# Optimization experiments

Measured on AMD Instinct MI355X. Metric: run time of the kernel, lower is better.

## Reference

```python
import jax, jax.numpy as jnp
import numpy as np

B, N, F_IN = 8, 256, 24
SLOPE = 0.01  # nn.LeakyReLU default negative_slope

def _leaky(x):
    return jnp.where(x >= 0, x, SLOPE * x)

def _adj(x, ws, bs):
    # AdjacencyMatrixPrediction (eval mode: dropout = identity, bn=False)
    # x: [B,N,F]; pairwise abs diff -> [B,N,N,F]; 1x1 convs == per-position matmuls
    h = jnp.abs(x[:, :, None, :] - x[:, None, :, :])
    for w, b in zip(ws[:4], bs[:4]):
        h = _leaky(h @ w + b)
    logits = (h @ ws[4] + bs[4])[..., 0]  # [B,N,N]
    n = x.shape[1]
    logits = logits - jnp.eye(n, dtype=logits.dtype) * 1e8  # mask diagonal
    return jax.nn.softmax(logits, axis=2)  # softmax over j (columns)

def _graph(a, x, w, b):
    # gmul with J2 operator = concat([I @ x, A @ x], -1), then Linear(J*F_in -> F_out)
    agg = jnp.concatenate([x, jnp.einsum('bij,bjf->bif', a, x)], axis=-1)
    return agg @ w.T + b

def setup_inputs():
    key = jax.random.key(0)
    ks = jax.random.split(key, 16)
    def mk(k, shape):
        return jax.random.normal(k, shape, jnp.float32) * 0.05
    ch0 = [24, 192, 192, 192, 96, 1]   # first AdjacencyMatrixPrediction conv chain
    ch1 = [72, 192, 192, 192, 96, 1]   # last AdjacencyMatrixPrediction (24 + 48 input)
    inp = {'x': jax.random.normal(ks[0], (B, N, F_IN), jnp.float32)}
    i = 1
    for pfx, ch in (('a0', ch0), ('a1', ch1)):
        for l in range(5):
            inp[f'{pfx}_w{l}'] = mk(ks[i], (ch[l], ch[l + 1])); i += 1
            inp[f'{pfx}_b{l}'] = jnp.zeros((ch[l + 1],), jnp.float32)
    inp['g0_w'] = mk(ks[i], (48, 48)); i += 1   # GraphModule(24 -> 48, J=2)
    inp['g0_b'] = jnp.zeros((48,), jnp.float32)
    inp['g1_w'] = mk(ks[i], (1, 144)); i += 1   # layer_last GraphModule(72 -> 1, J=2)
    inp['g1_b'] = jnp.zeros((1,), jnp.float32)
    return inp

def reference(x, a0_w0, a0_b0, a0_w1, a0_b1, a0_w2, a0_b2, a0_w3, a0_b3, a0_w4, a0_b4,
              a1_w0, a1_b0, a1_w1, a1_b1, a1_w2, a1_b2, a1_w3, a1_b3, a1_w4, a1_b4,
              g0_w, g0_b, g1_w, g1_b):
    a0 = _adj(x, [a0_w0, a0_w1, a0_w2, a0_w3, a0_w4], [a0_b0, a0_b1, a0_b2, a0_b3, a0_b4])
    x1 = _leaky(_graph(a0, x, g0_w, g0_b))
    xc = jnp.concatenate([x, x1], axis=-1)  # [B,N,72]
    a1 = _adj(xc, [a1_w0, a1_w1, a1_w2, a1_w3, a1_w4], [a1_b0, a1_b1, a1_b2, a1_b3, a1_b4])
    out = _graph(a1, xc, g1_w, g1_b)  # [B,N,1]
    # classifiers returned as [B,N,N,1] like the torch code
    return out, a0[..., None], a1[..., None]
```

## Files before the change

### kernel.cpp

```cpp
#include <hip/hip_runtime.h>

typedef __bf16 bf16x8 __attribute__((ext_vector_type(8)));
typedef float f32x4 __attribute__((ext_vector_type(4)));

__device__ __forceinline__ unsigned short f2b(float f) {
    union { float f; unsigned u; } c; c.f = f;
    unsigned u = c.u;
    return (unsigned short)((u + 0x7FFFu + ((u >> 16) & 1u)) >> 16);
}

__device__ __forceinline__ unsigned pack2(float v0, float v1) {
    union { __bf16 h[2]; unsigned u; } c;
    c.h[0] = (__bf16)v0; c.h[1] = (__bf16)v1;
    return c.u;
}

__device__ __forceinline__ void gload_lds16(const unsigned short* g, unsigned short* l) {
    __builtin_amdgcn_global_load_lds(
        (__attribute__((address_space(1))) unsigned int*)(g),
        (__attribute__((address_space(3))) unsigned int*)(l), 16, 0, 0);
}

template<int NFRAGS>
__device__ __forceinline__ void stage_frags(const unsigned short* __restrict__ g,
                                            unsigned short* l, int wid, int lane)
{
#pragma unroll
    for (int k = 0; k < (NFRAGS + 3) / 4; ++k) {
        const int idx = wid + k * 4;
        if ((NFRAGS % 4 == 0) || idx < NFRAGS)
            gload_lds16(g + idx * 512 + lane * 8, l + idx * 512);
    }
}

__device__ __forceinline__ void decode_entry(int e, int& b, int& i, int& j0, bool& offdiag)
{
    b = e / 1152;
    const int r = e - b * 1152;
    const int tp = r >> 5;
    const int row_in = r & 31;
    int rg = 0, tt = tp;
#pragma unroll 8
    for (;;) { int cnt = 8 - rg; if (tt < cnt) break; tt -= cnt; ++rg; }
    const int cg = rg + tt;
    i = rg * 32 + row_in;
    j0 = cg * 32;
    offdiag = (cg != rg);
}

template<int CIN, int KN0>
__device__ __forceinline__ void build_frags0(const float* __restrict__ xi,
    const float* __restrict__ xj, int cl, int g, bf16x8 (&B0)[2][6])
{
#pragma unroll
    for (int s = 0; s < KN0; ++s) {
        const int f0 = s * 32 + 8 * g;
        const bool valid = f0 < CIN;
        f32x4 xa = {0.f,0.f,0.f,0.f}, xb = {0.f,0.f,0.f,0.f};
        if (valid) { xa = *(const f32x4*)(xi + f0); xb = *(const f32x4*)(xi + f0 + 4); }
#pragma unroll
        for (int t = 0; t < 2; ++t) {
            bf16x8 r;
            if (valid) {
                const float* pj = xj + (16 * t + cl) * CIN + f0;
                f32x4 ja = *(const f32x4*)pj, jb = *(const f32x4*)(pj + 4);
#pragma unroll
                for (int e = 0; e < 4; ++e) {
                    r[e]     = (__bf16)fabsf(xa[e] - ja[e]);
                    r[e + 4] = (__bf16)fabsf(xb[e] - jb[e]);
                }
            } else {
#pragma unroll
                for (int e = 0; e < 8; ++e) r[e] = (__bf16)0.f;
            }
            B0[t][s] = r;
        }
    }
}

template<int KN, int CP>
__device__ __forceinline__ void run_cpair(const unsigned short* wlds,
    const float* __restrict__ bias, const bf16x8 (&Bc)[2][6], bf16x8 (&Bn)[2][6],
    int lane, int g)
{
    f32x4 acc[2][2];
#pragma unroll
    for (int cc = 0; cc < 2; ++cc) {
        f32x4 bv = *(const f32x4*)&bias[(2 * CP + cc) * 16 + 4 * g];
        acc[cc][0] = bv; acc[cc][1] = bv;
    }
#pragma unroll
    for (int s = 0; s < KN; ++s) {
#pragma unroll
        for (int cc = 0; cc < 2; ++cc) {
            bf16x8 w = *(const bf16x8*)&wlds[((cc * KN + s) * 64 + lane) * 8];
#pragma unroll
            for (int t = 0; t < 2; ++t)
                acc[cc][t] = __builtin_amdgcn_mfma_f32_16x16x32_bf16(w, Bc[t][s], acc[cc][t], 0, 0, 0);
        }
    }
#pragma unroll
    for (int t = 0; t < 2; ++t) {
        union { unsigned w[4]; bf16x8 v; } outv;
#pragma unroll
        for (int cc = 0; cc < 2; ++cc)
#pragma unroll
            for (int m = 0; m < 2; ++m) {
                float v0 = acc[cc][t][2 * m], v1 = acc[cc][t][2 * m + 1];
                v0 = fmaxf(v0, 0.01f * v0);
                v1 = fmaxf(v1, 0.01f * v1);
                outv.w[cc * 2 + m] = pack2(v0, v1);
            }
        Bn[t][CP] = outv.v;
    }
}

#define STEP(NF, OFF, ...) \
    stage_frags<NF>(wchain + (OFF), nxt, wid, lane); \
    __VA_ARGS__; \
    __syncthreads(); { unsigned short* tswp_ = cur; cur = nxt; nxt = tswp_; }

template<int CIN, int KN0>
__global__ __launch_bounds__(256, 3)
void adj_mlp_kernel(const float* __restrict__ src,
                    const unsigned short* __restrict__ wchain,
                    const unsigned short* __restrict__ w4f,
                    const float* __restrict__ b0, const float* __restrict__ b1,
                    const float* __restrict__ b2, const float* __restrict__ b3,
                    const float* __restrict__ b4,
                    float* __restrict__ logits)
{
    __shared__ unsigned short wbuf0[6144], wbuf1[6144];
    const int tid = threadIdx.x;
    const int wid = tid >> 6, lane = tid & 63;
    const int cl = lane & 15, g = lane >> 4;

    int b, i, j0; bool offdiag;
    decode_entry(blockIdx.x * 4 + wid, b, i, j0, offdiag);

    const float* xi = src + (b * 256 + i) * CIN;
    const float* xj = src + (b * 256 + j0) * CIN;

    const int CPSZ0 = 2 * KN0 * 512;
    const int B1 = 12 * KN0 * 512;
    const int B2 = B1 + 36864;
    const int B3 = B1 + 73728;
    const int CPSZ = 6144;

    stage_frags<2 * KN0>(wchain, wbuf0, wid, lane);

    bf16x8 Ba[2][6], Bb[2][6];
    build_frags0<CIN, KN0>(xi, xj, cl, g, Ba);
    __syncthreads();
    unsigned short* cur = wbuf0;
    unsigned short* nxt = wbuf1;

    STEP(2 * KN0, 1 * CPSZ0, run_cpair<KN0, 0>(cur, b0, Ba, Bb, lane, g))
    STEP(2 * KN0, 2 * CPSZ0, run_cpair<KN0, 1>(cur, b0, Ba, Bb, lane, g))
    STEP(2 * KN0, 3 * CPSZ0, run_cpair<KN0, 2>(cur, b0, Ba, Bb, lane, g))
    STEP(2 * KN0, 4 * CPSZ0, run_cpair<KN0, 3>(cur, b0, Ba, Bb, lane, g))
    STEP(2 * KN0, 5 * CPSZ0, run_cpair<KN0, 4>(cur, b0, Ba, Bb, lane, g))
    STEP(12, B1,             run_cpair<KN0, 5>(cur, b0, Ba, Bb, lane, g))
    STEP(12, B1 + 1 * CPSZ,  run_cpair<6, 0>(cur, b1, Bb, Ba, lane, g))
    STEP(12, B1 + 2 * CPSZ,  run_cpair<6, 1>(cur, b1, Bb, Ba, lane, g))
    STEP(12, B1 + 3 * CPSZ,  run_cpair<6, 2>(cur, b1, Bb, Ba, lane, g))
    STEP(12, B1 + 4 * CPSZ,  run_cpair<6, 3>(cur, b1, Bb, Ba, lane, g))
    STEP(12, B1 + 5 * CPSZ,  run_cpair<6, 4>(cur, b1, Bb, Ba, lane, g))
    STEP(12, B2,             run_cpair<6, 5>(cur, b1, Bb, Ba, lane, g))
    STEP(12, B2 + 1 * CPSZ,  run_cpair<6, 0>(cur, b2, Ba, Bb, lane, g))
    STEP(12, B2 + 2 * CPSZ,  run_cpair<6, 1>(cur, b2, Ba, Bb, lane, g))
    STEP(12, B2 + 3 * CPSZ,  run_cpair<6, 2>(cur, b2, Ba, Bb, lane, g))
    STEP(12, B2 + 4 * CPSZ,  run_cpair<6, 3>(cur, b2, Ba, Bb, lane, g))
    STEP(12, B2 + 5 * CPSZ,  run_cpair<6, 4>(cur, b2, Ba, Bb, lane, g))
    STEP(12, B3,             run_cpair<6, 5>(cur, b2, Ba, Bb, lane, g))
    STEP(12, B3 + 1 * CPSZ,  run_cpair<6, 0>(cur, b3, Bb, Ba, lane, g))
    STEP(12, B3 + 2 * CPSZ,  run_cpair<6, 1>(cur, b3, Bb, Ba, lane, g))
    run_cpair<6, 2>(cur, b3, Bb, Ba, lane, g);

    const float bv4 = b4[0];
#pragma unroll
    for (int t = 0; t < 2; ++t) {
        f32x4 acc = {bv4, bv4, bv4, bv4};
#pragma unroll
        for (int s = 0; s < 3; ++s) {
            bf16x8 w = *(const bf16x8*)(w4f + (s * 64 + lane) * 8);
            acc = __builtin_amdgcn_mfma_f32_16x16x32_bf16(w, Ba[t][s], acc, 0, 0, 0);
        }
        if (g == 0) {
            int j = j0 + 16 * t + cl;
            float lg = acc[0];
            if (j == i) lg -= 1e8f;
            logits[(b * 256 + i) * 256 + j] = lg;
            if (offdiag)
                logits[(b * 256 + j) * 256 + i] = lg;
        }
    }
}

struct PackPtrs { const float* w[10]; };

__global__ void pack_kernel(PackPtrs pp, unsigned short* __restrict__ dst)
{
    const int K_[10]   = {24, 192, 192, 192, 72, 192, 192, 192, 96, 96};
    const int KN_[10]  = {1, 6, 6, 6, 3, 6, 6, 6, 3, 3};
    const int NO_[10]  = {192, 192, 192, 96, 192, 192, 192, 96, 1, 1};
    const int OFF_[10] = {0, 6144, 43008, 79872, 98304, 116736, 153600, 190464, 208896, 210432};
    const int LEN_[10] = {6144, 36864, 36864, 18432, 18432, 36864, 36864, 18432, 1536, 1536};
    int t = blockIdx.x * 256 + threadIdx.x;
    int layer = 0, base = 0;
#pragma unroll
    for (int L = 0; L < 10; ++L)
        if (t >= base + LEN_[L]) { base += LEN_[L]; layer = L + 1; }
    if (layer >= 10) return;
    int u = t - base;
    int e = u & 7;
    int lane = (u >> 3) & 63;
    int gg = lane >> 4;
    int KN = KN_[layer];
    int fi = u >> 9;
    int s = fi % KN;
    int c = fi / KN;
    int k;
    if (layer == 0 || layer == 4)
        k = s * 32 + gg * 8 + e;
    else
        k = s * 32 + ((e >> 2) << 4) + (gg << 2) + (e & 3);
    int col = (c << 4) + (lane & 15);
    float v = 0.f;
    if (layer < 8) {
        if (k < K_[layer]) v = pp.w[layer][k * NO_[layer] + col];
    } else {
        if ((lane & 15) == 0) v = pp.w[layer][k];
    }
    dst[OFF_[layer] + u] = f2b(v);
}

template<int F>
__global__ __launch_bounds__(256)
void softmax_agg_kernel(float* __restrict__ amat, const float* __restrict__ src,
                        float* __restrict__ agg)
{
    __shared__ float pl[256];
    __shared__ float redm[4], reds[4];
    const int row = blockIdx.x;
    const int b = row >> 8;
    float* arow = amat + row * 256;
    const int t = threadIdx.x;
    const int lane = t & 63, wid = t >> 6;
    float v = arow[t];
    float m = v;
#pragma unroll
    for (int off = 32; off; off >>= 1) m = fmaxf(m, __shfl_xor(m, off));
    if (lane == 0) redm[wid] = m;
    __syncthreads();
    m = fmaxf(fmaxf(redm[0], redm[1]), fmaxf(redm[2], redm[3]));
    float e = __expf(v - m);
    float sum = e;
#pragma unroll
    for (int off = 32; off; off >>= 1) sum += __shfl_xor(sum, off);
    if (lane == 0) reds[wid] = sum;
    __syncthreads();
    sum = reds[0] + reds[1] + reds[2] + reds[3];
    float p = e / sum;
    arow[t] = p;
    pl[t] = p;
    __syncthreads();
    if (t < F) {
        const float* sb = src + (b * 256) * F + t;
        float acc = 0.f;
#pragma unroll 8
        for (int j = 0; j < 256; ++j)
            acc += pl[j] * sb[j * F];
        agg[row * F + t] = acc;
    }
}

__global__ __launch_bounds__(64)
void graph0_kernel(const float* __restrict__ x, const float* __restrict__ agg0,
                   const float* __restrict__ w, const float* __restrict__ bias,
                   float* __restrict__ xc)
{
    int row = blockIdx.x;
    int t = threadIdx.x;
    const float* xr = x + row * 24;
    const float* ar = agg0 + row * 24;
    if (t < 24) xc[row * 72 + t] = xr[t];
    if (t < 48) {
        float acc = bias[t];
#pragma unroll
        for (int f = 0; f < 24; ++f) acc += xr[f] * w[t * 48 + f];
#pragma unroll
        for (int f = 0; f < 24; ++f) acc += ar[f] * w[t * 48 + 24 + f];
        acc = acc >= 0.f ? acc : 0.01f * acc;
        xc[row * 72 + 24 + t] = acc;
    }
}

__global__ __launch_bounds__(64)
void graph1_kernel(const float* __restrict__ xc, const float* __restrict__ agg1,
                   const float* __restrict__ w, const float* __restrict__ bias,
                   float* __restrict__ out)
{
    int row = blockIdx.x;
    int t = threadIdx.x;
    float acc = 0.f;
    for (int idx = t; idx < 144; idx += 64) {
        float v = (idx < 72) ? xc[row * 72 + idx] : agg1[row * 72 + idx - 72];
        acc += v * w[idx];
    }
#pragma unroll
    for (int off = 32; off >= 1; off >>= 1) acc += __shfl_xor(acc, off);
    if (t == 0) out[row] = acc + bias[0];
}

extern "C" void kernel_launch(void* const* d_in, const int* in_sizes, int n_in,
                              void* d_out, int out_size, void* d_ws, size_t ws_size,
                              hipStream_t stream)
{
    const float* x = (const float*)d_in[0];
    float* out = (float*)d_out;
    float* a0 = out + 2048;
    float* a1 = a0 + 524288;

    char* ws = (char*)d_ws;
    unsigned short* packed = (unsigned short*)ws;
    float* xc   = (float*)(ws + 458752);
    float* agg0 = (float*)(ws + 1048576);
    float* agg1 = (float*)(ws + 1245184);

    PackPtrs pp;
    pp.w[0] = (const float*)d_in[1];
    pp.w[1] = (const float*)d_in[3];
    pp.w[2] = (const float*)d_in[5];
    pp.w[3] = (const float*)d_in[7];
    pp.w[4] = (const float*)d_in[11];
    pp.w[5] = (const float*)d_in[13];
    pp.w[6] = (const float*)d_in[15];
    pp.w[7] = (const float*)d_in[17];
    pp.w[8] = (const float*)d_in[9];
    pp.w[9] = (const float*)d_in[19];
    pack_kernel<<<828, 256, 0, stream>>>(pp, packed);

    adj_mlp_kernel<24, 1><<<2304, 256, 0, stream>>>(
        x, packed, packed + 208896,
        (const float*)d_in[2], (const float*)d_in[4], (const float*)d_in[6],
        (const float*)d_in[8], (const float*)d_in[10], a0);

    softmax_agg_kernel<24><<<2048, 256, 0, stream>>>(a0, x, agg0);

    graph0_kernel<<<2048, 64, 0, stream>>>(x, agg0,
        (const float*)d_in[21], (const float*)d_in[22], xc);

    adj_mlp_kernel<72, 3><<<2304, 256, 0, stream>>>(
        xc, packed + 98304, packed + 210432,
        (const float*)d_in[12], (const float*)d_in[14], (const float*)d_in[16],
        (const float*)d_in[18], (const float*)d_in[20], a1);

    softmax_agg_kernel<72><<<2048, 256, 0, stream>>>(a1, xc, agg1);

    graph1_kernel<<<2048, 64, 0, stream>>>(xc, agg1,
        (const float*)d_in[23], (const float*)d_in[24], out);
}
```

Measured before the change: 147.0 us.

## Stage uniform weight pages with split waitcnt barriers and batched layer-0 phases

Weight staging now always moves a full 6144-element page, so layer 0 (KN0=1 or 3) packs several channel pairs into each phase. The pipeline drops from 21 to 16 or 18 barrier steps. Each step's __syncthreads is replaced by inline-asm s_waitcnt vmcnt(3)+s_barrier before compute and lgkmcnt(0)+s_barrier after, so the prefetch of the next page can stay in flight while the current page is used. Bias is added after the MFMA accumulation instead of used as the initial accumulator. The hand-written waitcnt counts risk correctness if the compiler reorders or adds other vector-memory loads.

```diff
diff --git a/kernel.cpp b/kernel.cpp
--- a/kernel.cpp
+++ b/kernel.cpp
@@ -21,15 +21,13 @@
         (__attribute__((address_space(3))) unsigned int*)(l), 16, 0, 0);
 }
 
-template<int NFRAGS>
-__device__ __forceinline__ void stage_frags(const unsigned short* __restrict__ g,
-                                            unsigned short* l, int wid, int lane)
-{
-#pragma unroll
-    for (int k = 0; k < (NFRAGS + 3) / 4; ++k) {
+__device__ __forceinline__ void stage_page(const unsigned short* __restrict__ g,
+                                           unsigned short* l, int wid, int lane)
+{
+#pragma unroll
+    for (int k = 0; k < 3; ++k) {
         const int idx = wid + k * 4;
-        if ((NFRAGS % 4 == 0) || idx < NFRAGS)
-            gload_lds16(g + idx * 512 + lane * 8, l + idx * 512);
+        gload_lds16(g + idx * 512 + lane * 8, l + idx * 512);
     }
 }
 
@@ -83,12 +81,14 @@
     const float* __restrict__ bias, const bf16x8 (&Bc)[2][6], bf16x8 (&Bn)[2][6],
     int lane, int g)
 {
+    f32x4 bv0 = *(const f32x4*)&bias[(2 * CP + 0) * 16 + 4 * g];
+    f32x4 bv1 = *(const f32x4*)&bias[(2 * CP + 1) * 16 + 4 * g];
     f32x4 acc[2][2];
 #pragma unroll
-    for (int cc = 0; cc < 2; ++cc) {
-        f32x4 bv = *(const f32x4*)&bias[(2 * CP + cc) * 16 + 4 * g];
-        acc[cc][0] = bv; acc[cc][1] = bv;
-    }
+    for (int cc = 0; cc < 2; ++cc)
+#pragma unroll
+        for (int t = 0; t < 2; ++t)
+            acc[cc][t] = f32x4{0.f, 0.f, 0.f, 0.f};
 #pragma unroll
     for (int s = 0; s < KN; ++s) {
 #pragma unroll
@@ -103,22 +103,52 @@
     for (int t = 0; t < 2; ++t) {
         union { unsigned w[4]; bf16x8 v; } outv;
 #pragma unroll
-        for (int cc = 0; cc < 2; ++cc)
+        for (int cc = 0; cc < 2; ++cc) {
+            const f32x4 bv = cc ? bv1 : bv0;
 #pragma unroll
             for (int m = 0; m < 2; ++m) {
-                float v0 = acc[cc][t][2 * m], v1 = acc[cc][t][2 * m + 1];
+                float v0 = acc[cc][t][2 * m] + bv[2 * m];
+                float v1 = acc[cc][t][2 * m + 1] + bv[2 * m + 1];
                 v0 = fmaxf(v0, 0.01f * v0);
                 v1 = fmaxf(v1, 0.01f * v1);
                 outv.w[cc * 2 + m] = pack2(v0, v1);
             }
+        }
         Bn[t][CP] = outv.v;
     }
 }
 
-#define STEP(NF, OFF, ...) \
-    stage_frags<NF>(wchain + (OFF), nxt, wid, lane); \
+__device__ __forceinline__ void compute_l0_kn1(const unsigned short* cur,
+    const float* __restrict__ b0, const bf16x8 (&Ba)[2][6], bf16x8 (&Bb)[2][6],
+    int lane, int g)
+{
+    run_cpair<1, 0>(cur,        b0, Ba, Bb, lane, g);
+    run_cpair<1, 1>(cur + 1024, b0, Ba, Bb, lane, g);
+    run_cpair<1, 2>(cur + 2048, b0, Ba, Bb, lane, g);
+    run_cpair<1, 3>(cur + 3072, b0, Ba, Bb, lane, g);
+    run_cpair<1, 4>(cur + 4096, b0, Ba, Bb, lane, g);
+    run_cpair<1, 5>(cur + 5120, b0, Ba, Bb, lane, g);
+}
+
+template<int P2>
+__device__ __forceinline__ void compute_l0_kn3(const unsigned short* cur,
+    const float* __restrict__ b0, const bf16x8 (&Ba)[2][6], bf16x8 (&Bb)[2][6],
+    int lane, int g)
+{
+    run_cpair<3, 2 * P2>    (cur,        b0, Ba, Bb, lane, g);
+    run_cpair<3, 2 * P2 + 1>(cur + 3072, b0, Ba, Bb, lane, g);
+}
+
+#define PH(OFF, ...) \
+    stage_page(wchain + (OFF), nxt, wid, lane); \
+    asm volatile("s_waitcnt vmcnt(3)\n\ts_barrier" ::: "memory"); \
     __VA_ARGS__; \
-    __syncthreads(); { unsigned short* tswp_ = cur; cur = nxt; nxt = tswp_; }
+    asm volatile("s_waitcnt lgkmcnt(0)\n\ts_barrier" ::: "memory"); \
+    { unsigned short* t_ = cur; cur = nxt; nxt = t_; }
+
+#define PHLAST(...) \
+    asm volatile("s_waitcnt vmcnt(0)\n\ts_barrier" ::: "memory"); \
+    __VA_ARGS__;
 
 template<int CIN, int KN0>
 __global__ __launch_bounds__(256, 3)
@@ -141,41 +171,50 @@
     const float* xi = src + (b * 256 + i) * CIN;
     const float* xj = src + (b * 256 + j0) * CIN;
 
-    const int CPSZ0 = 2 * KN0 * 512;
-    const int B1 = 12 * KN0 * 512;
-    const int B2 = B1 + 36864;
-    const int B3 = B1 + 73728;
-    const int CPSZ = 6144;
-
-    stage_frags<2 * KN0>(wchain, wbuf0, wid, lane);
+    stage_page(wchain, wbuf0, wid, lane);
 
     bf16x8 Ba[2][6], Bb[2][6];
     build_frags0<CIN, KN0>(xi, xj, cl, g, Ba);
-    __syncthreads();
     unsigned short* cur = wbuf0;
     unsigned short* nxt = wbuf1;
 
-    STEP(2 * KN0, 1 * CPSZ0, run_cpair<KN0, 0>(cur, b0, Ba, Bb, lane, g))
-    STEP(2 * KN0, 2 * CPSZ0, run_cpair<KN0, 1>(cur, b0, Ba, Bb, lane, g))
-    STEP(2 * KN0, 3 * CPSZ0, run_cpair<KN0, 2>(cur, b0, Ba, Bb, lane, g))
-    STEP(2 * KN0, 4 * CPSZ0, run_cpair<KN0, 3>(cur, b0, Ba, Bb, lane, g))
-    STEP(2 * KN0, 5 * CPSZ0, run_cpair<KN0, 4>(cur, b0, Ba, Bb, lane, g))
-    STEP(12, B1,             run_cpair<KN0, 5>(cur, b0, Ba, Bb, lane, g))
-    STEP(12, B1 + 1 * CPSZ,  run_cpair<6, 0>(cur, b1, Bb, Ba, lane, g))
-    STEP(12, B1 + 2 * CPSZ,  run_cpair<6, 1>(cur, b1, Bb, Ba, lane, g))
-    STEP(12, B1 + 3 * CPSZ,  run_cpair<6, 2>(cur, b1, Bb, Ba, lane, g))
-    STEP(12, B1 + 4 * CPSZ,  run_cpair<6, 3>(cur, b1, Bb, Ba, lane, g))
-    STEP(12, B1 + 5 * CPSZ,  run_cpair<6, 4>(cur, b1, Bb, Ba, lane, g))
-    STEP(12, B2,             run_cpair<6, 5>(cur, b1, Bb, Ba, lane, g))
-    STEP(12, B2 + 1 * CPSZ,  run_cpair<6, 0>(cur, b2, Ba, Bb, lane, g))
-    STEP(12, B2 + 2 * CPSZ,  run_cpair<6, 1>(cur, b2, Ba, Bb, lane, g))
-    STEP(12, B2 + 3 * CPSZ,  run_cpair<6, 2>(cur, b2, Ba, Bb, lane, g))
-    STEP(12, B2 + 4 * CPSZ,  run_cpair<6, 3>(cur, b2, Ba, Bb, lane, g))
-    STEP(12, B2 + 5 * CPSZ,  run_cpair<6, 4>(cur, b2, Ba, Bb, lane, g))
-    STEP(12, B3,             run_cpair<6, 5>(cur, b2, Ba, Bb, lane, g))
-    STEP(12, B3 + 1 * CPSZ,  run_cpair<6, 0>(cur, b3, Bb, Ba, lane, g))
-    STEP(12, B3 + 2 * CPSZ,  run_cpair<6, 1>(cur, b3, Bb, Ba, lane, g))
-    run_cpair<6, 2>(cur, b3, Bb, Ba, lane, g);
+    if constexpr (KN0 == 1) {
+        PH( 1 * 6144, compute_l0_kn1(cur, b0, Ba, Bb, lane, g))
+        PH( 2 * 6144, run_cpair<6, 0>(cur, b1, Bb, Ba, lane, g))
+        PH( 3 * 6144, run_cpair<6, 1>(cur, b1, Bb, Ba, lane, g))
+        PH( 4 * 6144, run_cpair<6, 2>(cur, b1, Bb, Ba, lane, g))
+        PH( 5 * 6144, run_cpair<6, 3>(cur, b1, Bb, Ba, lane, g))
+        PH( 6 * 6144, run_cpair<6, 4>(cur, b1, Bb, Ba, lane, g))
+        PH( 7 * 6144, run_cpair<6, 5>(cur, b1, Bb, Ba, lane, g))
+        PH( 8 * 6144, run_cpair<6, 0>(cur, b2, Ba, Bb, lane, g))
+        PH( 9 * 6144, run_cpair<6, 1>(cur, b2, Ba, Bb, lane, g))
+        PH(10 * 6144, run_cpair<6, 2>(cur, b2, Ba, Bb, lane, g))
+        PH(11 * 6144, run_cpair<6, 3>(cur, b2, Ba, Bb, lane, g))
+        PH(12 * 6144, run_cpair<6, 4>(cur, b2, Ba, Bb, lane, g))
+        PH(13 * 6144, run_cpair<6, 5>(cur, b2, Ba, Bb, lane, g))
+        PH(14 * 6144, run_cpair<6, 0>(cur, b3, Bb, Ba, lane, g))
+        PH(15 * 6144, run_cpair<6, 1>(cur, b3, Bb, Ba, lane, g))
+        PHLAST(       run_cpair<6, 2>(cur, b3, Bb, Ba, lane, g))
+    } else {
+        PH( 1 * 6144, compute_l0_kn3<0>(cur, b0, Ba, Bb, lane, g))
+        PH( 2 * 6144, compute_l0_kn3<1>(cur, b0, Ba, Bb, lane, g))
+        PH( 3 * 6144, compute_l0_kn3<2>(cur, b0, Ba, Bb, lane, g))
+        PH( 4 * 6144, run_cpair<6, 0>(cur, b1, Bb, Ba, lane, g))
+        PH( 5 * 6144, run_cpair<6, 1>(cur, b1, Bb, Ba, lane, g))
+        PH( 6 * 6144, run_cpair<6, 2>(cur, b1, Bb, Ba, lane, g))
+        PH( 7 * 6144, run_cpair<6, 3>(cur, b1, Bb, Ba, lane, g))
+        PH( 8 * 6144, run_cpair<6, 4>(cur, b1, Bb, Ba, lane, g))
+        PH( 9 * 6144, run_cpair<6, 5>(cur, b1, Bb, Ba, lane, g))
+        PH(10 * 6144, run_cpair<6, 0>(cur, b2, Ba, Bb, lane, g))
+        PH(11 * 6144, run_cpair<6, 1>(cur, b2, Ba, Bb, lane, g))
+        PH(12 * 6144, run_cpair<6, 2>(cur, b2, Ba, Bb, lane, g))
+        PH(13 * 6144, run_cpair<6, 3>(cur, b2, Ba, Bb, lane, g))
+        PH(14 * 6144, run_cpair<6, 4>(cur, b2, Ba, Bb, lane, g))
+        PH(15 * 6144, run_cpair<6, 5>(cur, b2, Ba, Bb, lane, g))
+        PH(16 * 6144, run_cpair<6, 0>(cur, b3, Bb, Ba, lane, g))
+        PH(17 * 6144, run_cpair<6, 1>(cur, b3, Bb, Ba, lane, g))
+        PHLAST(       run_cpair<6, 2>(cur, b3, Bb, Ba, lane, g))
+    }
 
     const float bv4 = b4[0];
 #pragma unroll
```

Result: faster. 141.8 us (median of 2 runs) (-3.5%).
